# Performance work log

Measured on AMD Instinct MI355X. Metric: run time of the kernel, lower is better.

The kernel has to match this reference:

```python
import jax, jax.numpy as jnp
import numpy as np

B, N, F, FP, H = 4, 2048, 64, 32, 4
BN_EPS = 1e-3  # tf.layers.batch_normalization default


def setup_inputs() -> dict:
    key = jax.random.key(0)
    ks = jax.random.split(key, 8)
    x = jax.random.normal(ks[0], (B, N, F), dtype=jnp.float32)
    adj = jax.random.uniform(ks[1], (B, N, N), dtype=jnp.float32)
    attn_mask = jnp.zeros((B, N, N), dtype=jnp.float32)
    # per-head parameters stacked on leading head axis
    W = jax.random.normal(ks[2], (H, F, FP), dtype=jnp.float32) * 0.1
    a_self = jax.random.normal(ks[3], (H, FP), dtype=jnp.float32) * 0.1
    a_neigh = jax.random.normal(ks[4], (H, FP), dtype=jnp.float32) * 0.1
    bias = jnp.zeros((H, FP), dtype=jnp.float32)
    # batch-norm (inference) params over concat dim H*FP
    gamma = jnp.ones((H * FP,), dtype=jnp.float32)
    beta = jnp.zeros((H * FP,), dtype=jnp.float32)
    mov_mean = jnp.zeros((H * FP,), dtype=jnp.float32)
    mov_var = jnp.ones((H * FP,), dtype=jnp.float32)
    return dict(x=x, adj=adj, attn_mask=attn_mask, W=W, a_self=a_self,
                a_neigh=a_neigh, bias=bias, gamma=gamma, beta=beta,
                mov_mean=mov_mean, mov_var=mov_var)


def reference(x, adj, attn_mask, W, a_self, a_neigh, bias, gamma, beta,
              mov_mean, mov_var):
    # features per head: [B, H, N, FP]
    feats = jnp.einsum('bnf,hfd->bhnd', x, W)
    s = jnp.einsum('bhnd,hd->bhn', feats, a_self)    # attn_for_self
    t = jnp.einsum('bhnd,hd->bhn', feats, a_neigh)   # attn_for_neighs
    dense = s[..., :, None] + t[..., None, :]        # [B, H, N, N]
    dense = jnp.where(dense > 0, dense, 0.2 * dense)  # LeakyReLU(0.2)
    dense = dense + attn_mask[:, None]
    alpha = jax.nn.softmax(dense, axis=-1)
    alpha = alpha * adj[:, None]                     # include_ew=True
    # eval mode: dropout is identity
    node_feats = jnp.einsum('bhnm,bhmd->bhnd', alpha, feats) + bias[None, :, None, :]
    # attention stats losses
    nonz = (alpha != 0).sum(axis=-1)                 # [B, H, N]
    deg = (adj != 0).sum(axis=-1)                    # [B, N]
    uloss = jnp.sum(jnp.mean((nonz - deg[:, None, :]).astype(jnp.float32), axis=-1))
    eloss = jnp.sum(jnp.mean(jnp.sum(jnp.abs(alpha), axis=-1), axis=-1))
    # concat heads -> [B, N, H*FP]
    out = jnp.transpose(node_feats, (0, 2, 1, 3)).reshape(B, N, H * FP)
    # batch norm, inference mode
    out = (out - mov_mean) * jax.lax.rsqrt(mov_var + BN_EPS) * gamma + beta
    return jax.nn.relu(out), uloss, eloss
```

## Files before the change

### kernel.cpp

```cpp
#include <hip/hip_runtime.h>


#define B_ 4
#define N_ 2048
#define F_ 64
#define FP_ 32
#define H_ 4
#define C_ 128
#define IT_ 32
#define ITILES_ (N_ / IT_)
#define JCA_ 4
#define JSPANA_ (N_ / JCA_)
#define JST_ 64
#define NST_ (JSPANA_ / JST_)
#define LOG2E_ 1.44269504088896f

typedef __attribute__((ext_vector_type(8))) short short8v;
typedef __attribute__((ext_vector_type(4))) float f32x4;
typedef __attribute__((ext_vector_type(4))) int   int4v;

union PkU { int4v i; short8v s; };

extern "C" __device__ float __ocml_native_exp2_f32(float);

__device__ __forceinline__ float exp2fast(float x) {
#if __has_builtin(__builtin_amdgcn_exp2f)
    return __builtin_amdgcn_exp2f(x);
#else
    return __ocml_native_exp2_f32(x);
#endif
}

__device__ __forceinline__ unsigned short f2bf(float f) {
    unsigned u = __float_as_uint(f);
    u += 0x7fffu + ((u >> 16) & 1u);
    return (unsigned short)(u >> 16);
}

__device__ __forceinline__ void attn_qstep(
    float si, const float* av, const float* mv, const float* tv,
    float& l, float& A, int4v& apk)
{
#pragma unroll
    for (int qq = 0; qq < 4; ++qq) {
        float d0 = si + tv[2 * qq];
        d0 = fmaxf(d0, 0.2f * d0);
        d0 = fmaf(mv[2 * qq], LOG2E_, d0);
        float e0 = exp2fast(d0);
        float p0 = e0 * av[2 * qq];
        float d1 = si + tv[2 * qq + 1];
        d1 = fmaxf(d1, 0.2f * d1);
        d1 = fmaf(mv[2 * qq + 1], LOG2E_, d1);
        float e1 = exp2fast(d1);
        float p1 = e1 * av[2 * qq + 1];
        l += e0 + e1;
        A += p0 + p1;
        unsigned u0 = __float_as_uint(p0) + 0x8000u;
        unsigned u1 = __float_as_uint(p1) + 0x8000u;
        apk[qq] = (int)__builtin_amdgcn_perm(u1, u0, 0x07060302u);
    }
}

__device__ __forceinline__ void gl_lds16(const float* g, float* l) {
    __builtin_amdgcn_global_load_lds(
        (const __attribute__((address_space(1))) unsigned*)g,
        (__attribute__((address_space(3))) unsigned*)l, 16, 0, 0);
}

__global__ __launch_bounds__(256) void prep_kernel(
    const float* __restrict__ x, const float* __restrict__ W,
    const float* __restrict__ a_self, const float* __restrict__ a_neigh,
    unsigned short* __restrict__ featsT, float* __restrict__ sbuf,
    float* __restrict__ tbuf)
{
    int blk = blockIdx.x;
    int b = blk >> 6, nt = blk & 63;
    int n0 = nt << 5;
    int t = threadIdx.x, h = t >> 6, lane = t & 63;
    int quad = lane >> 4, col = lane & 15;

    short8v bw[2][2];
    const float* Wh = W + (size_t)h * F_ * FP_;
#pragma unroll
    for (int kc = 0; kc < 2; ++kc)
#pragma unroll
        for (int dt = 0; dt < 2; ++dt)
#pragma unroll
            for (int e = 0; e < 8; ++e) {
                int f = kc * 32 + quad * 8 + e;
                bw[kc][dt][e] = (short)f2bf(Wh[f * FP_ + dt * 16 + col]);
            }
    float as0 = a_self[h * FP_ + col],  as1 = a_self[h * FP_ + 16 + col];
    float an0 = a_neigh[h * FP_ + col], an1 = a_neigh[h * FP_ + 16 + col];
    size_t hrow = ((size_t)b * H_ + h) * N_;
    size_t ftb  = ((size_t)b * H_ + h) * FP_;

    for (int ms = 0; ms < 2; ++ms) {
        int row = n0 + ms * 16 + col;
        const float* xr = x + ((size_t)b * N_ + row) * F_;
        f32x4 acc0 = {0.f, 0.f, 0.f, 0.f}, acc1 = {0.f, 0.f, 0.f, 0.f};
#pragma unroll
        for (int kc = 0; kc < 2; ++kc) {
            float4 x0 = *(const float4*)(xr + kc * 32 + quad * 8);
            float4 x1 = *(const float4*)(xr + kc * 32 + quad * 8 + 4);
            short8v av;
            av[0] = (short)f2bf(x0.x); av[1] = (short)f2bf(x0.y);
            av[2] = (short)f2bf(x0.z); av[3] = (short)f2bf(x0.w);
            av[4] = (short)f2bf(x1.x); av[5] = (short)f2bf(x1.y);
            av[6] = (short)f2bf(x1.z); av[7] = (short)f2bf(x1.w);
            acc0 = __builtin_amdgcn_mfma_f32_16x16x32_bf16(av, bw[kc][0], acc0, 0, 0, 0);
            acc1 = __builtin_amdgcn_mfma_f32_16x16x32_bf16(av, bw[kc][1], acc1, 0, 0, 0);
        }
        {
            ushort4 v0, v1;
            v0.x = f2bf(acc0[0]); v0.y = f2bf(acc0[1]);
            v0.z = f2bf(acc0[2]); v0.w = f2bf(acc0[3]);
            v1.x = f2bf(acc1[0]); v1.y = f2bf(acc1[1]);
            v1.z = f2bf(acc1[2]); v1.w = f2bf(acc1[3]);
            size_t nidx = (size_t)n0 + ms * 16 + quad * 4;
            *(ushort4*)(featsT + (ftb + col) * N_ + nidx)      = v0;
            *(ushort4*)(featsT + (ftb + 16 + col) * N_ + nidx) = v1;
        }
#pragma unroll
        for (int rr = 0; rr < 4; ++rr) {
            float sv = acc0[rr] * as0 + acc1[rr] * as1;
            float tv = acc0[rr] * an0 + acc1[rr] * an1;
#pragma unroll
            for (int off = 8; off; off >>= 1) {
                sv += __shfl_down(sv, off);
                tv += __shfl_down(tv, off);
            }
            if (col == 0) {
                int n = n0 + ms * 16 + quad * 4 + rr;
                sbuf[hrow + n] = sv * LOG2E_;
                tbuf[hrow + n] = tv * LOG2E_;
            }
        }
    }
}

__global__ __launch_bounds__(256, 4) void attn_kernel(
    const float* __restrict__ adj, const float* __restrict__ msk,
    const unsigned short* __restrict__ featsT,
    const float* __restrict__ sbuf, const float* __restrict__ tbuf,
    float* __restrict__ part, float* __restrict__ lpart)
{
    __shared__ __align__(16) float ladj[2][IT_ * JST_];
    __shared__ __align__(16) float lmsk[2][IT_ * JST_];
    __shared__ __align__(16) float lt[2][H_ * JST_];

    const int blk = blockIdx.x;
    const int jc = blk & (JCA_ - 1);
    const int it = (blk >> 2) & (ITILES_ - 1);
    const int b  = blk >> 8;
    const int t = threadIdx.x, h = t >> 6, lane = t & 63;
    const int quad = lane >> 4, r = lane & 15;
    const int i0 = it * IT_;
    const int jbase = jc * JSPANA_;

    size_t hrow = ((size_t)b * H_ + h) * N_;
    float si0 = sbuf[hrow + i0 + r];
    float si1 = sbuf[hrow + i0 + 16 + r];
    const unsigned short* ft0 = featsT + (((size_t)b * H_ + h) * FP_ + r) * N_
                                + jbase + quad * 8;
    const unsigned short* ft1 = ft0 + (size_t)16 * N_;

    const float* asrc[2];
    const float* msrc[2];
#pragma unroll
    for (int ii = 0; ii < 2; ++ii) {
        int row = 8 * h + 4 * ii + (lane >> 4);
        int cs = ((lane & 15) ^ (row & 7)) << 2;
        size_t go = ((size_t)b * N_ + i0 + row) * N_ + jbase + cs;
        asrc[ii] = adj + go;
        msrc[ii] = msk + go;
    }
    const float* tsrc = tbuf + ((size_t)b * H_ + (lane >> 4)) * N_
                        + jbase + ((lane & 15) << 2);

    f32x4 acc00 = {0.f,0.f,0.f,0.f}, acc01 = {0.f,0.f,0.f,0.f};
    f32x4 acc10 = {0.f,0.f,0.f,0.f}, acc11 = {0.f,0.f,0.f,0.f};
    float l0 = 0.f, A0 = 0.f, l1 = 0.f, A1 = 0.f;

    auto STAGE = [&](int bf, int st) {
        const int j0 = st * JST_;
#pragma unroll
        for (int ii = 0; ii < 2; ++ii) {
            gl_lds16(asrc[ii] + j0, &ladj[bf][(8 * h + 4 * ii) * JST_]);
            gl_lds16(msrc[ii] + j0, &lmsk[bf][(8 * h + 4 * ii) * JST_]);
        }
        if (h == 0) gl_lds16(tsrc + j0, &lt[bf][0]);
    };

    STAGE(0, 0);
    __syncthreads();

    for (int st = 0; st < NST_; ++st) {
        const int bf = st & 1;
        if (st + 1 < NST_) STAGE(bf ^ 1, st + 1);
        const int jg = st * JST_;
#pragma unroll
        for (int kc = 0; kc < 2; ++kc) {
            const int jt = kc * 32 + quad * 8;
            const int g0 = (jt >> 2) ^ (r & 7);
            const int g1 = ((jt >> 2) + 1) ^ (r & 7);
            const int s0 = g0 << 2, s1 = g1 << 2;
            float4 a0l = *(const float4*)&ladj[bf][r * JST_ + s0];
            float4 a0h = *(const float4*)&ladj[bf][r * JST_ + s1];
            float4 a1l = *(const float4*)&ladj[bf][(r + 16) * JST_ + s0];
            float4 a1h = *(const float4*)&ladj[bf][(r + 16) * JST_ + s1];
            float4 m0l = *(const float4*)&lmsk[bf][r * JST_ + s0];
            float4 m0h = *(const float4*)&lmsk[bf][r * JST_ + s1];
            float4 m1l = *(const float4*)&lmsk[bf][(r + 16) * JST_ + s0];
            float4 m1h = *(const float4*)&lmsk[bf][(r + 16) * JST_ + s1];
            float4 t0 = *(const float4*)&lt[bf][h * JST_ + jt];
            float4 t1 = *(const float4*)&lt[bf][h * JST_ + jt + 4];
            float tv[8] = {t0.x, t0.y, t0.z, t0.w, t1.x, t1.y, t1.z, t1.w};
            short8v bv0 = *(const short8v*)(ft0 + jg + kc * 32);
            short8v bv1 = *(const short8v*)(ft1 + jg + kc * 32);
            PkU ap0, ap1;
            {
                float av[8] = {a0l.x,a0l.y,a0l.z,a0l.w,a0h.x,a0h.y,a0h.z,a0h.w};
                float mv[8] = {m0l.x,m0l.y,m0l.z,m0l.w,m0h.x,m0h.y,m0h.z,m0h.w};
                attn_qstep(si0, av, mv, tv, l0, A0, ap0.i);
            }
            {
                float av[8] = {a1l.x,a1l.y,a1l.z,a1l.w,a1h.x,a1h.y,a1h.z,a1h.w};
                float mv[8] = {m1l.x,m1l.y,m1l.z,m1l.w,m1h.x,m1h.y,m1h.z,m1h.w};
                attn_qstep(si1, av, mv, tv, l1, A1, ap1.i);
            }
            acc00 = __builtin_amdgcn_mfma_f32_16x16x32_bf16(ap0.s, bv0, acc00, 0, 0, 0);
            acc01 = __builtin_amdgcn_mfma_f32_16x16x32_bf16(ap0.s, bv1, acc01, 0, 0, 0);
            acc10 = __builtin_amdgcn_mfma_f32_16x16x32_bf16(ap1.s, bv0, acc10, 0, 0, 0);
            acc11 = __builtin_amdgcn_mfma_f32_16x16x32_bf16(ap1.s, bv1, acc11, 0, 0, 0);
        }
        __syncthreads();
    }

    l0 += __shfl_down(l0, 32); l0 += __shfl_down(l0, 16);
    l1 += __shfl_down(l1, 32); l1 += __shfl_down(l1, 16);
    A0 += __shfl_down(A0, 32); A0 += __shfl_down(A0, 16);
    A1 += __shfl_down(A1, 32); A1 += __shfl_down(A1, 16);

    size_t pb = (((size_t)(b * H_ + h) * ITILES_ + it) * JCA_ + jc) * 1024;
    *(f32x4*)&part[pb + lane * 4]       = acc00;
    *(f32x4*)&part[pb + 256 + lane * 4] = acc01;
    *(f32x4*)&part[pb + 512 + lane * 4] = acc10;
    *(f32x4*)&part[pb + 768 + lane * 4] = acc11;
    if (lane < 16) {
        size_t lb = (((size_t)(b * H_ + h) * ITILES_ + it) * JCA_ + jc) * 64;
        lpart[lb + lane]      = l0;
        lpart[lb + 16 + lane] = l1;
        lpart[lb + 32 + lane] = A0;
        lpart[lb + 48 + lane] = A1;
    }
}

__global__ __launch_bounds__(256) void final_kernel(
    const float* __restrict__ part, const float* __restrict__ lpart,
    const float* __restrict__ bias, const float* __restrict__ gamma,
    const float* __restrict__ beta, const float* __restrict__ mmean,
    const float* __restrict__ mvar, float* __restrict__ lossbuf,
    float* __restrict__ out)
{
    __shared__ float ldsl[H_ * IT_];
    __shared__ float ldso[IT_ * 132];
    int blk = blockIdx.x;
    int b = blk >> 6, it = blk & 63;
    int t = threadIdx.x, h = t >> 6, lane = t & 63;
    int quad = lane >> 4, col = lane & 15;

    size_t pb = (((size_t)(b * H_ + h) * ITILES_ + it) * JCA_) * 1024;
    f32x4 C[4];
#pragma unroll
    for (int k = 0; k < 4; ++k) C[k] = (f32x4){0.f, 0.f, 0.f, 0.f};
#pragma unroll
    for (int c = 0; c < JCA_; ++c)
#pragma unroll
        for (int k = 0; k < 4; ++k)
            C[k] += *(const f32x4*)&part[pb + c * 1024 + k * 256 + lane * 4];

    size_t lb = (((size_t)(b * H_ + h) * ITILES_ + it) * JCA_) * 64;
    if (lane < 32) {
        float lt = 0.f, At = 0.f;
#pragma unroll
        for (int c = 0; c < JCA_; ++c) {
            lt += lpart[lb + c * 64 + lane];
            At += lpart[lb + c * 64 + 32 + lane];
        }
        ldsl[h * IT_ + lane] = lt;
        float e = At / lt;
#pragma unroll
        for (int off = 16; off; off >>= 1) e += __shfl_down(e, off);
        if (lane == 0) lossbuf[blk * H_ + h] = e;
    }
    __syncthreads();
#pragma unroll
    for (int dt = 0; dt < 2; ++dt) {
        int c = h * FP_ + dt * 16 + col;
        float sc = rsqrtf(mvar[c] + 1e-3f) * gamma[c];
        float sh = beta[c] - mmean[c] * sc;
        float bi = bias[c];
#pragma unroll
        for (int rr = 0; rr < 2; ++rr) {
            f32x4 Cv = C[rr * 2 + dt];
#pragma unroll
            for (int rrr = 0; rrr < 4; ++rrr) {
                int row = rr * 16 + quad * 4 + rrr;
                float node = Cv[rrr] / ldsl[h * IT_ + row] + bi;
                float o = node * sc + sh;
                ldso[row * 132 + c] = o > 0.f ? o : 0.f;
            }
        }
    }
    __syncthreads();
#pragma unroll
    for (int ps = 0; ps < 4; ++ps) {
        int s = ps * 256 + t;
        int row = s >> 5, c4 = (s & 31) * 4;
        *(float4*)(out + ((size_t)b * N_ + it * IT_ + row) * C_ + c4) =
            *(const float4*)&ldso[row * 132 + c4];
    }
}

__global__ __launch_bounds__(256) void loss_kernel(
    const float* __restrict__ lossbuf, float* __restrict__ out)
{
    float e = 0.f;
    for (int idx = threadIdx.x; idx < B_ * ITILES_ * H_; idx += 256)
        e += lossbuf[idx];
    __shared__ float se[256];
    se[threadIdx.x] = e;
    __syncthreads();
    for (int o = 128; o; o >>= 1) {
        if (threadIdx.x < o) se[threadIdx.x] += se[threadIdx.x + o];
        __syncthreads();
    }
    if (threadIdx.x == 0) {
        out[(size_t)B_ * N_ * C_]     = 0.f;
        out[(size_t)B_ * N_ * C_ + 1] = se[0] * (1.f / N_);
    }
}

extern "C" void kernel_launch(void* const* d_in, const int* in_sizes, int n_in,
                              void* d_out, int out_size, void* d_ws, size_t ws_size,
                              hipStream_t stream)
{
    const float* x         = (const float*)d_in[0];
    const float* adj       = (const float*)d_in[1];
    const float* attn_mask = (const float*)d_in[2];
    const float* W         = (const float*)d_in[3];
    const float* a_self    = (const float*)d_in[4];
    const float* a_neigh   = (const float*)d_in[5];
    const float* bias      = (const float*)d_in[6];
    const float* gamma     = (const float*)d_in[7];
    const float* beta      = (const float*)d_in[8];
    const float* mmean     = (const float*)d_in[9];
    const float* mvar      = (const float*)d_in[10];
    float* out = (float*)d_out;

    float* ws = (float*)d_ws;
    unsigned short* featsT = (unsigned short*)ws;
    float* sbuf  = ws + 524288;
    float* tbuf  = sbuf + (size_t)B_ * H_ * N_;
    float* part  = tbuf + (size_t)B_ * H_ * N_;
    float* lpart = part + (size_t)B_ * H_ * ITILES_ * JCA_ * 1024;
    float* lossb = lpart + (size_t)B_ * H_ * ITILES_ * JCA_ * 64;

    hipLaunchKernelGGL(prep_kernel, dim3(B_ * 64), dim3(256), 0, stream,
                       x, W, a_self, a_neigh, featsT, sbuf, tbuf);
    hipLaunchKernelGGL(attn_kernel, dim3(B_ * ITILES_ * JCA_), dim3(256), 0, stream,
                       adj, attn_mask, featsT, sbuf, tbuf, part, lpart);
    hipLaunchKernelGGL(final_kernel, dim3(B_ * ITILES_), dim3(256), 0, stream,
                       part, lpart, bias, gamma, beta, mmean, mvar,
                       lossb, out);
    hipLaunchKernelGGL(loss_kernel, dim3(1), dim3(256), 0, stream,
                       lossb, out);
}
```

Measured before the change: 189.0 us.

## Software-pipeline featsT register prefetch with explicit vmcnt waits and barriers

The attention loop is restructured into a two-buffer ping-pong. The bf16 featsT operands for the next stage are loaded into registers one stage ahead, and the full __syncthreads is replaced by s_waitcnt vmcnt(4) plus s_barrier. The wait only drains the LDS-bound adjacency, mask and t loads, so the register prefetch stays in flight across the barrier. The t-vector LDS staging is also spread across all four waves instead of wave 0. This relies on the hand-counted vmcnt matching the exact number of memory operations issued per wave, which is fragile if the compiler reorders or splits loads.

```diff
diff --git a/kernel.cpp b/kernel.cpp
--- a/kernel.cpp
+++ b/kernel.cpp
@@ -67,6 +67,8 @@
         (__attribute__((address_space(3))) unsigned*)l, 16, 0, 0);
 }
 
+#define WAITV(N) asm volatile("s_waitcnt vmcnt(" #N ")" ::: "memory")
+
 __global__ __launch_bounds__(256) void prep_kernel(
     const float* __restrict__ x, const float* __restrict__ W,
     const float* __restrict__ a_self, const float* __restrict__ a_neigh,
@@ -175,7 +177,7 @@
         asrc[ii] = adj + go;
         msrc[ii] = msk + go;
     }
-    const float* tsrc = tbuf + ((size_t)b * H_ + (lane >> 4)) * N_
+    const float* tsrc = tbuf + ((size_t)b * H_ + h) * N_
                         + jbase + ((lane & 15) << 2);
 
     f32x4 acc00 = {0.f,0.f,0.f,0.f}, acc01 = {0.f,0.f,0.f,0.f};
@@ -189,16 +191,16 @@
             gl_lds16(asrc[ii] + j0, &ladj[bf][(8 * h + 4 * ii) * JST_]);
             gl_lds16(msrc[ii] + j0, &lmsk[bf][(8 * h + 4 * ii) * JST_]);
         }
-        if (h == 0) gl_lds16(tsrc + j0, &lt[bf][0]);
+        if (lane < 16) gl_lds16(tsrc + j0, &lt[bf][h * JST_]);
     };
-
-    STAGE(0, 0);
-    __syncthreads();
-
-    for (int st = 0; st < NST_; ++st) {
-        const int bf = st & 1;
-        if (st + 1 < NST_) STAGE(bf ^ 1, st + 1);
+    auto LDBV = [&](short8v bv[2][2], int st) {
         const int jg = st * JST_;
+        bv[0][0] = *(const short8v*)(ft0 + jg);
+        bv[0][1] = *(const short8v*)(ft1 + jg);
+        bv[1][0] = *(const short8v*)(ft0 + jg + 32);
+        bv[1][1] = *(const short8v*)(ft1 + jg + 32);
+    };
+    auto COMPUTE = [&](int bf, short8v bv[2][2]) {
 #pragma unroll
         for (int kc = 0; kc < 2; ++kc) {
             const int jt = kc * 32 + quad * 8;
@@ -216,8 +218,6 @@
             float4 t0 = *(const float4*)&lt[bf][h * JST_ + jt];
             float4 t1 = *(const float4*)&lt[bf][h * JST_ + jt + 4];
             float tv[8] = {t0.x, t0.y, t0.z, t0.w, t1.x, t1.y, t1.z, t1.w};
-            short8v bv0 = *(const short8v*)(ft0 + jg + kc * 32);
-            short8v bv1 = *(const short8v*)(ft1 + jg + kc * 32);
             PkU ap0, ap1;
             {
                 float av[8] = {a0l.x,a0l.y,a0l.z,a0l.w,a0h.x,a0h.y,a0h.z,a0h.w};
@@ -229,12 +229,37 @@
                 float mv[8] = {m1l.x,m1l.y,m1l.z,m1l.w,m1h.x,m1h.y,m1h.z,m1h.w};
                 attn_qstep(si1, av, mv, tv, l1, A1, ap1.i);
             }
-            acc00 = __builtin_amdgcn_mfma_f32_16x16x32_bf16(ap0.s, bv0, acc00, 0, 0, 0);
-            acc01 = __builtin_amdgcn_mfma_f32_16x16x32_bf16(ap0.s, bv1, acc01, 0, 0, 0);
-            acc10 = __builtin_amdgcn_mfma_f32_16x16x32_bf16(ap1.s, bv0, acc10, 0, 0, 0);
-            acc11 = __builtin_amdgcn_mfma_f32_16x16x32_bf16(ap1.s, bv1, acc11, 0, 0, 0);
-        }
-        __syncthreads();
+            acc00 = __builtin_amdgcn_mfma_f32_16x16x32_bf16(ap0.s, bv[kc][0], acc00, 0, 0, 0);
+            acc01 = __builtin_amdgcn_mfma_f32_16x16x32_bf16(ap0.s, bv[kc][1], acc01, 0, 0, 0);
+            acc10 = __builtin_amdgcn_mfma_f32_16x16x32_bf16(ap1.s, bv[kc][0], acc10, 0, 0, 0);
+            acc11 = __builtin_amdgcn_mfma_f32_16x16x32_bf16(ap1.s, bv[kc][1], acc11, 0, 0, 0);
+        }
+    };
+
+    short8v bvA[2][2], bvB[2][2];
+    STAGE(0, 0);
+    __builtin_amdgcn_sched_barrier(0);
+    LDBV(bvA, 0);
+    WAITV(4);
+    __builtin_amdgcn_s_barrier();
+
+    for (int sp = 0; sp < NST_; sp += 2) {
+        STAGE(1, sp + 1);
+        __builtin_amdgcn_sched_barrier(0);
+        LDBV(bvB, sp + 1);
+        COMPUTE(0, bvA);
+        WAITV(4);
+        __builtin_amdgcn_s_barrier();
+        if (sp + 2 < NST_) {
+            STAGE(0, sp + 2);
+            __builtin_amdgcn_sched_barrier(0);
+            LDBV(bvA, sp + 2);
+            COMPUTE(1, bvB);
+            WAITV(4);
+            __builtin_amdgcn_s_barrier();
+        } else {
+            COMPUTE(1, bvB);
+        }
     }
 
     l0 += __shfl_down(l0, 32); l0 += __shfl_down(l0, 16);
```

After: 224.4 us. 1.19x slower.

## Load adj/mask/t directly from global into registers, dropping LDS staging

Applied to the files above, without the earlier changes.

Removes the double-buffered LDS staging of adjacency, mask and t tiles via global_load_lds, along with the per-stage barriers. Each lane now reads its own 8 contiguous floats per row straight from global memory in a flat loop unrolled by two. This cuts LDS traffic, synchronisation and LDS occupancy pressure. In exchange, the four heads (waves) each reload the same adj/mask rows from global/L2 instead of sharing one staged copy, and there is no explicit prefetch.

```diff
diff --git a/kernel.cpp b/kernel.cpp
--- a/kernel.cpp
+++ b/kernel.cpp
@@ -11,8 +11,6 @@
 #define ITILES_ (N_ / IT_)
 #define JCA_ 4
 #define JSPANA_ (N_ / JCA_)
-#define JST_ 64
-#define NST_ (JSPANA_ / JST_)
 #define LOG2E_ 1.44269504088896f
 
 typedef __attribute__((ext_vector_type(8))) short short8v;
@@ -61,12 +59,6 @@
     }
 }
 
-__device__ __forceinline__ void gl_lds16(const float* g, float* l) {
-    __builtin_amdgcn_global_load_lds(
-        (const __attribute__((address_space(1))) unsigned*)g,
-        (__attribute__((address_space(3))) unsigned*)l, 16, 0, 0);
-}
-
 __global__ __launch_bounds__(256) void prep_kernel(
     const float* __restrict__ x, const float* __restrict__ W,
     const float* __restrict__ a_self, const float* __restrict__ a_neigh,
@@ -145,10 +137,6 @@
     const float* __restrict__ sbuf, const float* __restrict__ tbuf,
     float* __restrict__ part, float* __restrict__ lpart)
 {
-    __shared__ __align__(16) float ladj[2][IT_ * JST_];
-    __shared__ __align__(16) float lmsk[2][IT_ * JST_];
-    __shared__ __align__(16) float lt[2][H_ * JST_];
-
     const int blk = blockIdx.x;
     const int jc = blk & (JCA_ - 1);
     const int it = (blk >> 2) & (ITILES_ - 1);
@@ -156,85 +144,55 @@
     const int t = threadIdx.x, h = t >> 6, lane = t & 63;
     const int quad = lane >> 4, r = lane & 15;
     const int i0 = it * IT_;
-    const int jbase = jc * JSPANA_;
+    const int jbase = jc * JSPANA_ + quad * 8;
 
     size_t hrow = ((size_t)b * H_ + h) * N_;
     float si0 = sbuf[hrow + i0 + r];
     float si1 = sbuf[hrow + i0 + 16 + r];
     const unsigned short* ft0 = featsT + (((size_t)b * H_ + h) * FP_ + r) * N_
-                                + jbase + quad * 8;
+                                + jbase;
     const unsigned short* ft1 = ft0 + (size_t)16 * N_;
-
-    const float* asrc[2];
-    const float* msrc[2];
-#pragma unroll
-    for (int ii = 0; ii < 2; ++ii) {
-        int row = 8 * h + 4 * ii + (lane >> 4);
-        int cs = ((lane & 15) ^ (row & 7)) << 2;
-        size_t go = ((size_t)b * N_ + i0 + row) * N_ + jbase + cs;
-        asrc[ii] = adj + go;
-        msrc[ii] = msk + go;
-    }
-    const float* tsrc = tbuf + ((size_t)b * H_ + (lane >> 4)) * N_
-                        + jbase + ((lane & 15) << 2);
+    const float* ar0 = adj + ((size_t)b * N_ + i0 + r) * N_ + jbase;
+    const float* ar1 = ar0 + (size_t)16 * N_;
+    const float* mr0 = msk + ((size_t)b * N_ + i0 + r) * N_ + jbase;
+    const float* mr1 = mr0 + (size_t)16 * N_;
+    const float* tp  = tbuf + hrow + jbase;
 
     f32x4 acc00 = {0.f,0.f,0.f,0.f}, acc01 = {0.f,0.f,0.f,0.f};
     f32x4 acc10 = {0.f,0.f,0.f,0.f}, acc11 = {0.f,0.f,0.f,0.f};
     float l0 = 0.f, A0 = 0.f, l1 = 0.f, A1 = 0.f;
 
-    auto STAGE = [&](int bf, int st) {
-        const int j0 = st * JST_;
-#pragma unroll
-        for (int ii = 0; ii < 2; ++ii) {
-            gl_lds16(asrc[ii] + j0, &ladj[bf][(8 * h + 4 * ii) * JST_]);
-            gl_lds16(msrc[ii] + j0, &lmsk[bf][(8 * h + 4 * ii) * JST_]);
-        }
-        if (h == 0) gl_lds16(tsrc + j0, &lt[bf][0]);
-    };
-
-    STAGE(0, 0);
-    __syncthreads();
-
-    for (int st = 0; st < NST_; ++st) {
-        const int bf = st & 1;
-        if (st + 1 < NST_) STAGE(bf ^ 1, st + 1);
-        const int jg = st * JST_;
-#pragma unroll
-        for (int kc = 0; kc < 2; ++kc) {
-            const int jt = kc * 32 + quad * 8;
-            const int g0 = (jt >> 2) ^ (r & 7);
-            const int g1 = ((jt >> 2) + 1) ^ (r & 7);
-            const int s0 = g0 << 2, s1 = g1 << 2;
-            float4 a0l = *(const float4*)&ladj[bf][r * JST_ + s0];
-            float4 a0h = *(const float4*)&ladj[bf][r * JST_ + s1];
-            float4 a1l = *(const float4*)&ladj[bf][(r + 16) * JST_ + s0];
-            float4 a1h = *(const float4*)&ladj[bf][(r + 16) * JST_ + s1];
-            float4 m0l = *(const float4*)&lmsk[bf][r * JST_ + s0];
-            float4 m0h = *(const float4*)&lmsk[bf][r * JST_ + s1];
-            float4 m1l = *(const float4*)&lmsk[bf][(r + 16) * JST_ + s0];
-            float4 m1h = *(const float4*)&lmsk[bf][(r + 16) * JST_ + s1];
-            float4 t0 = *(const float4*)&lt[bf][h * JST_ + jt];
-            float4 t1 = *(const float4*)&lt[bf][h * JST_ + jt + 4];
-            float tv[8] = {t0.x, t0.y, t0.z, t0.w, t1.x, t1.y, t1.z, t1.w};
-            short8v bv0 = *(const short8v*)(ft0 + jg + kc * 32);
-            short8v bv1 = *(const short8v*)(ft1 + jg + kc * 32);
-            PkU ap0, ap1;
-            {
-                float av[8] = {a0l.x,a0l.y,a0l.z,a0l.w,a0h.x,a0h.y,a0h.z,a0h.w};
-                float mv[8] = {m0l.x,m0l.y,m0l.z,m0l.w,m0h.x,m0h.y,m0h.z,m0h.w};
-                attn_qstep(si0, av, mv, tv, l0, A0, ap0.i);
-            }
-            {
-                float av[8] = {a1l.x,a1l.y,a1l.z,a1l.w,a1h.x,a1h.y,a1h.z,a1h.w};
-                float mv[8] = {m1l.x,m1l.y,m1l.z,m1l.w,m1h.x,m1h.y,m1h.z,m1h.w};
-                attn_qstep(si1, av, mv, tv, l1, A1, ap1.i);
-            }
-            acc00 = __builtin_amdgcn_mfma_f32_16x16x32_bf16(ap0.s, bv0, acc00, 0, 0, 0);
-            acc01 = __builtin_amdgcn_mfma_f32_16x16x32_bf16(ap0.s, bv1, acc01, 0, 0, 0);
-            acc10 = __builtin_amdgcn_mfma_f32_16x16x32_bf16(ap1.s, bv0, acc10, 0, 0, 0);
-            acc11 = __builtin_amdgcn_mfma_f32_16x16x32_bf16(ap1.s, bv1, acc11, 0, 0, 0);
-        }
-        __syncthreads();
+#pragma unroll 2
+    for (int kk = 0; kk < JSPANA_ / 32; ++kk) {
+        const int off = kk * 32;
+        float4 a0l = *(const float4*)(ar0 + off);
+        float4 a0h = *(const float4*)(ar0 + off + 4);
+        float4 a1l = *(const float4*)(ar1 + off);
+        float4 a1h = *(const float4*)(ar1 + off + 4);
+        float4 m0l = *(const float4*)(mr0 + off);
+        float4 m0h = *(const float4*)(mr0 + off + 4);
+        float4 m1l = *(const float4*)(mr1 + off);
+        float4 m1h = *(const float4*)(mr1 + off + 4);
+        float4 t0  = *(const float4*)(tp + off);
+        float4 t1  = *(const float4*)(tp + off + 4);
+        short8v bv0 = *(const short8v*)(ft0 + off);
+        short8v bv1 = *(const short8v*)(ft1 + off);
+        float tvv[8] = {t0.x, t0.y, t0.z, t0.w, t1.x, t1.y, t1.z, t1.w};
+        PkU ap0, ap1;
+        {
+            float avv[8] = {a0l.x,a0l.y,a0l.z,a0l.w,a0h.x,a0h.y,a0h.z,a0h.w};
+            float mvv[8] = {m0l.x,m0l.y,m0l.z,m0l.w,m0h.x,m0h.y,m0h.z,m0h.w};
+            attn_qstep(si0, avv, mvv, tvv, l0, A0, ap0.i);
+        }
+        {
+            float avv[8] = {a1l.x,a1l.y,a1l.z,a1l.w,a1h.x,a1h.y,a1h.z,a1h.w};
+            float mvv[8] = {m1l.x,m1l.y,m1l.z,m1l.w,m1h.x,m1h.y,m1h.z,m1h.w};
+            attn_qstep(si1, avv, mvv, tvv, l1, A1, ap1.i);
+        }
+        acc00 = __builtin_amdgcn_mfma_f32_16x16x32_bf16(ap0.s, bv0, acc00, 0, 0, 0);
+        acc01 = __builtin_amdgcn_mfma_f32_16x16x32_bf16(ap0.s, bv1, acc01, 0, 0, 0);
+        acc10 = __builtin_amdgcn_mfma_f32_16x16x32_bf16(ap1.s, bv0, acc10, 0, 0, 0);
+        acc11 = __builtin_amdgcn_mfma_f32_16x16x32_bf16(ap1.s, bv1, acc11, 0, 0, 0);
     }
 
     l0 += __shfl_down(l0, 32); l0 += __shfl_down(l0, 16);
```

Result: slower. 240.6 us (+27.3%).
